# Optimization experiments

Hardware: AMD Instinct MI355X
Metric: run time of the kernel (lower is better)

## Reference

```python
import jax, jax.numpy as jnp
import numpy as np

B = 8192; N = 50; NUM_NODES = 200000; NUM_EDGES = 1000000
FEAT = 64; EFEAT = 4; TD = 16; D = 64


def setup_inputs() -> dict:
    key = jax.random.key(0)
    ks = jax.random.split(key, 32)
    p = lambda i, shape: jax.random.normal(ks[i], shape, jnp.float32) * 0.05
    inp = {}
    nf = jax.random.normal(ks[0], (NUM_NODES, FEAT), jnp.float32)
    skills = jax.random.randint(ks[1], (NUM_NODES,), 0, 100).astype(jnp.float32)
    inp['node_raw_features'] = nf.at[:, 0].set(skills)  # col 0 = skill id
    inp['edge_raw_features'] = jax.random.normal(ks[2], (NUM_EDGES, EFEAT), jnp.float32)
    inp['src_node_ids'] = jax.random.randint(ks[3], (B,), 0, NUM_NODES)
    inp['dst_node_ids'] = jax.random.randint(ks[4], (B,), 0, NUM_NODES)
    inp['node_interact_times'] = jax.random.uniform(ks[5], (B,), jnp.float32, 0.0, 1e4)
    inp['src_neighbor_node_ids'] = jax.random.randint(ks[6], (B, N), 0, NUM_NODES)
    inp['src_neighbor_edge_ids'] = jax.random.randint(ks[7], (B, N), 0, NUM_EDGES)
    inp['src_neighbor_times'] = jax.random.uniform(ks[8], (B, N), jnp.float32, 0.0, 1e4)
    inp['dst_neighbor_node_ids'] = jax.random.randint(ks[9], (B, N), 0, NUM_NODES)
    inp['dst_neighbor_edge_ids'] = jax.random.randint(ks[10], (B, N), 0, NUM_EDGES)
    inp['dst_neighbor_times'] = jax.random.uniform(ks[11], (B, N), jnp.float32, 0.0, 1e4)
    # projection layers
    inp['W_feat'] = p(12, (FEAT, D)); inp['b_feat'] = p(13, (D,))
    inp['W_edge'] = p(14, (1, D));    inp['b_edge'] = p(15, (D,))
    inp['W_time'] = p(16, (TD, D));   inp['b_time'] = p(17, (D,))
    inp['W_struct'] = p(18, (1, D));  inp['b_struct'] = p(19, (D,))
    inp['W_out'] = p(20, (D, D));     inp['b_out'] = p(21, (D,))
    # time encoder (cos(w*dt + b), trainable Linear(1, TD) as in TGN TimeEncoder)
    inp['time_w'] = p(22, (TD,)); inp['time_b'] = p(23, (TD,))
    # src / dst GRUs (PyTorch layout: W_ih [3H,E], W_hh [3H,H])
    inp['src_W_ih'] = p(24, (3 * D, D)); inp['src_W_hh'] = p(25, (3 * D, D))
    inp['src_b_ih'] = p(26, (3 * D,));   inp['src_b_hh'] = p(27, (3 * D,))
    inp['dst_W_ih'] = p(28, (3 * D, D)); inp['dst_W_hh'] = p(29, (3 * D, D))
    inp['dst_b_ih'] = p(30, (3 * D,));   inp['dst_b_hh'] = p(31, (3 * D,))
    return inp


def _lin(x, W, b):
    return x @ W + b


def _gru_last_hidden(x, W_ih, W_hh, b_ih, b_hh):
    # x: [B, T, E] -> final hidden state [B, H] (PyTorch GRU equations)
    Bb, _, _ = x.shape
    H = W_hh.shape[1]

    def step(h, xt):
        gi = xt @ W_ih.T + b_ih            # [B, 3H]
        gh = h @ W_hh.T + b_hh             # [B, 3H]
        ir, iz, inn = jnp.split(gi, 3, axis=-1)
        hr, hz, hn = jnp.split(gh, 3, axis=-1)
        r = jax.nn.sigmoid(ir + hr)
        z = jax.nn.sigmoid(iz + hz)
        n = jnp.tanh(inn + r * hn)
        h_new = (1.0 - z) * n + z * h
        return h_new, None

    h0 = jnp.zeros((Bb, H), x.dtype)
    hT, _ = jax.lax.scan(step, h0, jnp.swapaxes(x, 0, 1))
    return hT


def reference(node_raw_features, edge_raw_features, src_node_ids, dst_node_ids,
              node_interact_times, src_neighbor_node_ids, src_neighbor_edge_ids,
              src_neighbor_times, dst_neighbor_node_ids, dst_neighbor_edge_ids,
              dst_neighbor_times, W_feat, b_feat, W_edge, b_edge, W_time, b_time,
              W_struct, b_struct, W_out, b_out, time_w, time_b,
              src_W_ih, src_W_hh, src_b_ih, src_b_hh,
              dst_W_ih, dst_W_hh, dst_b_ih, dst_b_hh):
    t = node_interact_times
    # append the query interaction itself (edge id 0) -> [B, N+1]
    src_nids = jnp.concatenate([src_neighbor_node_ids, src_node_ids[:, None]], 1)
    src_eids = jnp.concatenate([src_neighbor_edge_ids, jnp.zeros_like(src_node_ids)[:, None]], 1)
    src_ts = jnp.concatenate([src_neighbor_times, t[:, None]], 1)
    dst_nids = jnp.concatenate([dst_neighbor_node_ids, dst_node_ids[:, None]], 1)
    dst_eids = jnp.concatenate([dst_neighbor_edge_ids, jnp.zeros_like(dst_node_ids)[:, None]], 1)
    dst_ts = jnp.concatenate([dst_neighbor_times, t[:, None]], 1)

    # co-occurrence features [B, N, 1]
    co_src = (src_neighbor_node_ids == dst_node_ids[:, None]).astype(jnp.float32)[..., None]
    co_dst = (dst_neighbor_node_ids == src_node_ids[:, None]).astype(jnp.float32)[..., None]
    # skill match features [B, N, 1]
    src_skill = node_raw_features[src_nids][:, :-1, 0].astype(jnp.int32)
    dst_skill = node_raw_features[dst_nids][:, -1, 0].astype(jnp.int32)[:, None]
    skill_f = (src_skill == dst_skill).astype(jnp.float32)[..., None]

    src_struct = _lin(co_src, W_struct, b_struct)
    dst_struct = _lin(co_dst, W_struct, b_struct)
    skill_struct = _lin(skill_f, W_struct, b_struct)

    def get_feats(nids, eids, ts):
        node_f = _lin(node_raw_features[nids], W_feat, b_feat)        # [B,N+1,D]
        delta = t[:, None] - ts                                       # dual-decay ablation: delta times
        tenc = jnp.cos(delta[..., None] * time_w + time_b)            # [B,N+1,TD]
        time_f = _lin(tenc, W_time, b_time)                           # [B,N+1,D]
        edge_f = _lin(edge_raw_features[eids][..., :1], W_edge, b_edge)
        return node_f, edge_f, time_f

    sn, se, st = get_feats(src_nids, src_eids, src_ts)
    dn, de, dt = get_feats(dst_nids, dst_eids, dst_ts)
    src_feats = sn + se + st
    dst_feats = dn + de + dt

    src_emb = _gru_last_hidden(src_feats[:, :-1] + skill_struct + src_struct,
                               src_W_ih, src_W_hh, src_b_ih, src_b_hh) + (se + st)[:, -1]
    dst_emb = _gru_last_hidden((de + dt)[:, :-1] + dst_struct,
                               dst_W_ih, dst_W_hh, dst_b_ih, dst_b_hh) + dst_feats[:, -1]

    return _lin(src_emb, W_out, b_out), _lin(dst_emb, W_out, b_out)
```

## Files before the change

kernel.cpp:

```cpp
#include <hip/hip_runtime.h>
#include <stdint.h>

#define BB 8192
#define NN 50

typedef _Float16 half8 __attribute__((ext_vector_type(8)));
typedef float floatx4 __attribute__((ext_vector_type(4)));

union FragU { uint4 u; half8 h; };
static __device__ __forceinline__ half8 u2h(uint4 u) { FragU f; f.u = u; return f.h; }

static __device__ __forceinline__ uint32_t pk2u(float a, float b) {
    auto p = __builtin_amdgcn_cvt_pkrtz(a, b);
    uint32_t u; __builtin_memcpy(&u, &p, 4); return u;
}

#define MFMA(A, B, C) __builtin_amdgcn_mfma_f32_16x16x32_f16((A), (B), (C), 0, 0, 0)

static __device__ __forceinline__ float frcp(float x) {
#if __has_builtin(__builtin_amdgcn_rcpf)
    return __builtin_amdgcn_rcpf(x);
#else
    return 1.0f / x;
#endif
}
static __device__ __forceinline__ float fexp2(float x) {
#if __has_builtin(__builtin_amdgcn_exp2f)
    return __builtin_amdgcn_exp2f(x);
#else
    return __expf(0.69314718056f * x);
#endif
}

static __device__ __forceinline__ void bar_lds() {
    asm volatile("s_waitcnt lgkmcnt(0)" ::: "memory");
    __builtin_amdgcn_s_barrier();
}

__global__ __launch_bounds__(128, 2)
void dygkt7(const float* __restrict__ nodef, const float* __restrict__ edgef,
            const int* __restrict__ src_ids, const int* __restrict__ dst_ids,
            const float* __restrict__ times,
            const int* __restrict__ s_nids, const int* __restrict__ s_eids,
            const float* __restrict__ s_ts,
            const int* __restrict__ d_nids, const int* __restrict__ d_eids,
            const float* __restrict__ d_ts,
            const float* __restrict__ W_feat, const float* __restrict__ b_feat,
            const float* __restrict__ W_edge, const float* __restrict__ b_edge,
            const float* __restrict__ W_time, const float* __restrict__ b_time,
            const float* __restrict__ W_str,  const float* __restrict__ b_str,
            const float* __restrict__ W_out,  const float* __restrict__ b_out,
            const float* __restrict__ time_w, const float* __restrict__ time_b,
            const float* __restrict__ sWih, const float* __restrict__ sWhh,
            const float* __restrict__ sbih, const float* __restrict__ sbhh,
            const float* __restrict__ dWih, const float* __restrict__ dWhh,
            const float* __restrict__ dbih, const float* __restrict__ dbhh,
            float* __restrict__ out)
{
    __shared__ __align__(16) _Float16 xls[2][16 * 72];
    __shared__ __align__(16) _Float16 hls[2][16 * 72];
    __shared__ uint4 wihL[2][12][64];

    const int tid = threadIdx.x, w = tid >> 6, lane = tid & 63;
    const int g = lane >> 4, i16 = lane & 15;
    const bool is_src = (blockIdx.x & 1) == 0;
    const int b = (int)(blockIdx.x >> 1) * 16 + i16;

    const float SRZ = -1.44269504089f;
    const float SN  =  2.88539008178f;

    for (int q = tid; q < 16 * 72 / 2; q += 128) ((uint32_t*)hls[0])[q] = 0u;

    uint4 wf[2][2];
    #pragma unroll
    for (int tq = 0; tq < 2; ++tq)
        #pragma unroll
        for (int kh = 0; kh < 2; ++kh) {
            float v[8];
            #pragma unroll
            for (int j = 0; j < 8; ++j)
                v[j] = W_feat[(32 * kh + 8 * g + j) * 64 + 16 * (2 * w + tq) + i16];
            wf[tq][kh] = make_uint4(pk2u(v[0],v[1]), pk2u(v[2],v[3]), pk2u(v[4],v[5]), pk2u(v[6],v[7]));
        }

    const float* WI = is_src ? sWih : dWih;
    const float* WH = is_src ? sWhh : dWhh;
    uint4 whh[6][2];
    #pragma unroll
    for (int gt = 0; gt < 3; ++gt) {
        const float s = (gt == 2) ? SN : SRZ;
        #pragma unroll
        for (int tq = 0; tq < 2; ++tq)
            #pragma unroll
            for (int kh = 0; kh < 2; ++kh) {
                int row = 64 * gt + 16 * (2 * w + tq) + i16;
                const float* p = WI + (size_t)row * 64 + 32 * kh + 8 * g;
                float4 a = *(const float4*)p, c = *(const float4*)(p + 4);
                wihL[w][gt * 4 + tq * 2 + kh][lane] =
                    make_uint4(pk2u(s*a.x,s*a.y), pk2u(s*a.z,s*a.w), pk2u(s*c.x,s*c.y), pk2u(s*c.z,s*c.w));
                const float* qq = WH + (size_t)row * 64 + 32 * kh + 8 * g;
                float4 e = *(const float4*)qq, f = *(const float4*)(qq + 4);
                whh[gt * 2 + tq][kh] =
                    make_uint4(pk2u(s*e.x,s*e.y), pk2u(s*e.z,s*e.w), pk2u(s*f.x,s*f.y), pk2u(s*f.z,s*f.w));
            }
    }

    uint4 wtA[2];
    #pragma unroll
    for (int tq = 0; tq < 2; ++tq) {
        int mt = 2 * w + tq;
        float v[8];
        #pragma unroll
        for (int j = 0; j < 8; ++j) {
            int k = 8 * g + j, dim = 16 * mt + i16;
            float x = 0.0f;
            if (k < 16)       x = W_time[k * 64 + dim];
            else if (k == 16) x = W_edge[dim];
            else if (k == 17) x = W_str[dim];
            else if (k == 18) x = b_edge[dim] + b_time[dim];
            else if (k == 19) x = is_src ? (b_feat[dim] + 2.0f * b_str[dim]) : b_str[dim];
            else if (k == 20) x = b_feat[dim];
            v[j] = x;
        }
        wtA[tq] = make_uint4(pk2u(v[0],v[1]), pk2u(v[2],v[3]), pk2u(v[4],v[5]), pk2u(v[6],v[7]));
    }

    const float* BI = is_src ? sbih : dbih;
    const float* BH = is_src ? sbhh : dbhh;
    floatx4 brz[4], bin[2], bhn[2];
    #pragma unroll
    for (int gz = 0; gz < 2; ++gz)
        #pragma unroll
        for (int tq = 0; tq < 2; ++tq) {
            int r0 = 64 * gz + 16 * (2 * w + tq) + 4 * g;
            floatx4 v;
            #pragma unroll
            for (int r = 0; r < 4; ++r) v[r] = SRZ * (BI[r0 + r] + BH[r0 + r]);
            brz[gz * 2 + tq] = v;
        }
    #pragma unroll
    for (int tq = 0; tq < 2; ++tq) {
        int r0 = 128 + 16 * (2 * w + tq) + 4 * g;
        floatx4 vi, vh;
        #pragma unroll
        for (int r = 0; r < 4; ++r) { vi[r] = SN * BI[r0 + r]; vh[r] = SN * BH[r0 + r]; }
        bin[tq] = vi; bhn[tq] = vh;
    }

    const int* pn = (is_src ? s_nids : d_nids) + (size_t)b * NN;
    const int* pe = (is_src ? s_eids : d_eids) + (size_t)b * NN;
    const float* pt = (is_src ? s_ts : d_ts) + (size_t)b * NN;
    const float tqL = times[b];
    const int didL = dst_ids[b];
    const int oid = is_src ? didL : src_ids[b];
    const float dskill = is_src ? nodef[(size_t)didL * 64] : 0.0f;
    float twc[8], tbc[8];
    #pragma unroll
    for (int j = 0; j < 8; ++j) {
        int k = 8 * (g & 1) + j;
        twc[j] = time_w[k]; tbc[j] = time_b[k];
    }

    __syncthreads();

    int nidC = pn[0], eidC = pe[0];
    float tsC = pt[0];
    float e0C = edgef[4 * (size_t)eidC];
    float4 nfa = {0,0,0,0}, nfb = {0,0,0,0}, nfc = {0,0,0,0}, nfd = {0,0,0,0};
    if (is_src) {
        const float* rp = nodef + (size_t)nidC * 64 + 8 * g;
        nfa = *(const float4*)rp;        nfb = *(const float4*)(rp + 4);
        nfc = *(const float4*)(rp + 32); nfd = *(const float4*)(rp + 36);
    }
    int nidN = pn[1], eidN = pe[1];
    float tsN = pt[1];
    float e0N = edgef[4 * (size_t)eidN];
    float4 na = {0,0,0,0}, nb = {0,0,0,0}, nc = {0,0,0,0}, nd = {0,0,0,0};
    if (is_src) {
        const float* rp = nodef + (size_t)nidN * 64 + 8 * g;
        na = *(const float4*)rp;        nb = *(const float4*)(rp + 4);
        nc = *(const float4*)(rp + 32); nd = *(const float4*)(rp + 36);
    }

    const floatx4 z4 = {0,0,0,0};
    floatx4 gr[2], gz_[2], gn[2];
    floatx4 hM[2] = {{0,0,0,0},{0,0,0,0}};

    {
        float nsk = __shfl(nfa.x, i16);
        float sf = ((nidC == oid) ? 1.0f : 0.0f) +
                   ((is_src && nsk == dskill) ? 1.0f : 0.0f);
        float delta = tqL - tsC;
        uint4 tb4;
        if (g < 2) {
            float cv[8];
            #pragma unroll
            for (int j = 0; j < 8; ++j) cv[j] = __cosf(delta * twc[j] + tbc[j]);
            tb4 = make_uint4(pk2u(cv[0],cv[1]), pk2u(cv[2],cv[3]), pk2u(cv[4],cv[5]), pk2u(cv[6],cv[7]));
        } else if (g == 2) {
            tb4 = make_uint4(pk2u(e0C, sf), pk2u(1.0f, 1.0f), 0u, 0u);
        } else {
            tb4 = make_uint4(0u, 0u, 0u, 0u);
        }
        half8 tB = u2h(tb4);
        #pragma unroll
        for (int tq = 0; tq < 2; ++tq) {
            floatx4 xacc;
            if (is_src) {
                uint4 nf0 = make_uint4(pk2u(nfa.x,nfa.y), pk2u(nfa.z,nfa.w), pk2u(nfb.x,nfb.y), pk2u(nfb.z,nfb.w));
                uint4 nf1 = make_uint4(pk2u(nfc.x,nfc.y), pk2u(nfc.z,nfc.w), pk2u(nfd.x,nfd.y), pk2u(nfd.z,nfd.w));
                floatx4 a = MFMA(u2h(wf[tq][0]), u2h(nf0), z4);
                a = MFMA(u2h(wf[tq][1]), u2h(nf1), a);
                xacc = MFMA(u2h(wtA[tq]), tB, a);
            } else {
                xacc = MFMA(u2h(wtA[tq]), tB, z4);
            }
            *(uint2*)&xls[0][i16 * 72 + 32 * w + 16 * tq + 4 * g] =
                make_uint2(pk2u(xacc[0], xacc[1]), pk2u(xacc[2], xacc[3]));
        }
        bar_lds();
        half8 xB0 = u2h(*(const uint4*)&xls[0][i16 * 72 + 8 * g]);
        half8 xB1 = u2h(*(const uint4*)&xls[0][i16 * 72 + 32 + 8 * g]);
        #pragma unroll
        for (int tq = 0; tq < 2; ++tq) {
            floatx4 a = MFMA(u2h(wihL[w][0 + tq * 2 + 0][lane]), xB0, brz[tq]);
            gr[tq]    = MFMA(u2h(wihL[w][0 + tq * 2 + 1][lane]), xB1, a);
            floatx4 c = MFMA(u2h(wihL[w][4 + tq * 2 + 0][lane]), xB0, brz[2 + tq]);
            gz_[tq]   = MFMA(u2h(wihL[w][4 + tq * 2 + 1][lane]), xB1, c);
            floatx4 e = MFMA(u2h(wihL[w][8 + tq * 2 + 0][lane]), xB0, bin[tq]);
            gn[tq]    = MFMA(u2h(wihL[w][8 + tq * 2 + 1][lane]), xB1, e);
        }
    }

    int cur = 0;
    for (int t = 0; t < NN; ++t) {
        const bool hasx = (t + 1 < NN);

        nidC = nidN; eidC = eidN; tsC = tsN; e0C = e0N;
        nfa = na; nfb = nb; nfc = nc; nfd = nd;

        if (hasx) {
            float nsk = __shfl(nfa.x, i16);
            float sf = ((nidC == oid) ? 1.0f : 0.0f) +
                       ((is_src && nsk == dskill) ? 1.0f : 0.0f);
            float delta = tqL - tsC;
            uint4 tb4;
            if (g < 2) {
                float cv[8];
                #pragma unroll
                for (int j = 0; j < 8; ++j) cv[j] = __cosf(delta * twc[j] + tbc[j]);
                tb4 = make_uint4(pk2u(cv[0],cv[1]), pk2u(cv[2],cv[3]), pk2u(cv[4],cv[5]), pk2u(cv[6],cv[7]));
            } else if (g == 2) {
                tb4 = make_uint4(pk2u(e0C, sf), pk2u(1.0f, 1.0f), 0u, 0u);
            } else {
                tb4 = make_uint4(0u, 0u, 0u, 0u);
            }
            half8 tB = u2h(tb4);
            #pragma unroll
            for (int tq = 0; tq < 2; ++tq) {
                floatx4 xacc;
                if (is_src) {
                    uint4 nf0 = make_uint4(pk2u(nfa.x,nfa.y), pk2u(nfa.z,nfa.w), pk2u(nfb.x,nfb.y), pk2u(nfb.z,nfb.w));
                    uint4 nf1 = make_uint4(pk2u(nfc.x,nfc.y), pk2u(nfc.z,nfc.w), pk2u(nfd.x,nfd.y), pk2u(nfd.z,nfd.w));
                    floatx4 a = MFMA(u2h(wf[tq][0]), u2h(nf0), z4);
                    a = MFMA(u2h(wf[tq][1]), u2h(nf1), a);
                    xacc = MFMA(u2h(wtA[tq]), tB, a);
                } else {
                    xacc = MFMA(u2h(wtA[tq]), tB, z4);
                }
                *(uint2*)&xls[cur ^ 1][i16 * 72 + 32 * w + 16 * tq + 4 * g] =
                    make_uint2(pk2u(xacc[0], xacc[1]), pk2u(xacc[2], xacc[3]));
            }
        }

        if (t + 2 < NN) {
            nidN = pn[t + 2]; eidN = pe[t + 2]; tsN = pt[t + 2];
            e0N = edgef[4 * (size_t)eidN];
            if (is_src) {
                const float* rp = nodef + (size_t)nidN * 64 + 8 * g;
                na = *(const float4*)rp;        nb = *(const float4*)(rp + 4);
                nc = *(const float4*)(rp + 32); nd = *(const float4*)(rp + 36);
            }
        }

        bar_lds();

        half8 hB0 = u2h(*(const uint4*)&hls[cur][i16 * 72 + 8 * g]);
        half8 hB1 = u2h(*(const uint4*)&hls[cur][i16 * 72 + 32 + 8 * g]);

        floatx4 rg[2], zg[2], ha[2];
        #pragma unroll
        for (int tq = 0; tq < 2; ++tq) {
            floatx4 a = MFMA(u2h(whh[tq][0]), hB0, gr[tq]);
            rg[tq]    = MFMA(u2h(whh[tq][1]), hB1, a);
            floatx4 c = MFMA(u2h(whh[2 + tq][0]), hB0, gz_[tq]);
            zg[tq]    = MFMA(u2h(whh[2 + tq][1]), hB1, c);
            floatx4 e = MFMA(u2h(whh[4 + tq][0]), hB0, bhn[tq]);
            ha[tq]    = MFMA(u2h(whh[4 + tq][1]), hB1, e);
        }

        #pragma unroll
        for (int tq = 0; tq < 2; ++tq)
            #pragma unroll
            for (int r = 0; r < 4; ++r) {
                float rr = frcp(1.0f + fexp2(rg[tq][r]));
                float zz = frcp(1.0f + fexp2(zg[tq][r]));
                float vv = gn[tq][r] + rr * ha[tq][r];
                float nn = 1.0f - 2.0f * frcp(fexp2(vv) + 1.0f);
                hM[tq][r] = nn + zz * (hM[tq][r] - nn);
            }

        #pragma unroll
        for (int tq = 0; tq < 2; ++tq)
            *(uint2*)&hls[cur ^ 1][i16 * 72 + 32 * w + 16 * tq + 4 * g] =
                make_uint2(pk2u(hM[tq][0], hM[tq][1]), pk2u(hM[tq][2], hM[tq][3]));

        if (hasx) {
            half8 xB0 = u2h(*(const uint4*)&xls[cur ^ 1][i16 * 72 + 8 * g]);
            half8 xB1 = u2h(*(const uint4*)&xls[cur ^ 1][i16 * 72 + 32 + 8 * g]);
            #pragma unroll
            for (int tq = 0; tq < 2; ++tq) {
                floatx4 a = MFMA(u2h(wihL[w][0 + tq * 2 + 0][lane]), xB0, brz[tq]);
                gr[tq]    = MFMA(u2h(wihL[w][0 + tq * 2 + 1][lane]), xB1, a);
                floatx4 c = MFMA(u2h(wihL[w][4 + tq * 2 + 0][lane]), xB0, brz[2 + tq]);
                gz_[tq]   = MFMA(u2h(wihL[w][4 + tq * 2 + 1][lane]), xB1, c);
                floatx4 e = MFMA(u2h(wihL[w][8 + tq * 2 + 0][lane]), xB0, bin[tq]);
                gn[tq]    = MFMA(u2h(wihL[w][8 + tq * 2 + 1][lane]), xB1, e);
            }
        }

        cur ^= 1;
    }

    float e00 = edgef[0];
    uint4 tt4;
    if (g < 2) {
        float cv[8];
        #pragma unroll
        for (int j = 0; j < 8; ++j) cv[j] = __cosf(tbc[j]);
        tt4 = make_uint4(pk2u(cv[0],cv[1]), pk2u(cv[2],cv[3]), pk2u(cv[4],cv[5]), pk2u(cv[6],cv[7]));
    } else if (g == 2) {
        tt4 = make_uint4(pk2u(e00, 0.0f), pk2u(1.0f, 0.0f), pk2u(is_src ? 0.0f : 1.0f, 0.0f), 0u);
    } else {
        tt4 = make_uint4(0u, 0u, 0u, 0u);
    }
    half8 tT = u2h(tt4);

    floatx4 tacc[2];
    #pragma unroll
    for (int tq = 0; tq < 2; ++tq) tacc[tq] = MFMA(u2h(wtA[tq]), tT, z4);
    if (!is_src) {
        const float* rp = nodef + (size_t)didL * 64 + 8 * g;
        float4 da = *(const float4*)rp,        db = *(const float4*)(rp + 4);
        float4 dc = *(const float4*)(rp + 32), dd = *(const float4*)(rp + 36);
        uint4 d0 = make_uint4(pk2u(da.x,da.y), pk2u(da.z,da.w), pk2u(db.x,db.y), pk2u(db.z,db.w));
        uint4 d1 = make_uint4(pk2u(dc.x,dc.y), pk2u(dc.z,dc.w), pk2u(dd.x,dd.y), pk2u(dd.z,dd.w));
        #pragma unroll
        for (int tq = 0; tq < 2; ++tq) {
            tacc[tq] = MFMA(u2h(wf[tq][0]), u2h(d0), tacc[tq]);
            tacc[tq] = MFMA(u2h(wf[tq][1]), u2h(d1), tacc[tq]);
        }
    }

    uint4 wo[2][2];
    #pragma unroll
    for (int tq = 0; tq < 2; ++tq)
        #pragma unroll
        for (int kh = 0; kh < 2; ++kh) {
            float v[8];
            #pragma unroll
            for (int j = 0; j < 8; ++j)
                v[j] = W_out[(32 * kh + 8 * g + j) * 64 + 16 * (2 * w + tq) + i16];
            wo[tq][kh] = make_uint4(pk2u(v[0],v[1]), pk2u(v[2],v[3]), pk2u(v[4],v[5]), pk2u(v[6],v[7]));
        }

    #pragma unroll
    for (int tq = 0; tq < 2; ++tq) {
        floatx4 e = hM[tq] + tacc[tq];
        *(uint2*)&xls[0][i16 * 72 + 32 * w + 16 * tq + 4 * g] =
            make_uint2(pk2u(e[0], e[1]), pk2u(e[2], e[3]));
    }
    bar_lds();
    half8 eB0 = u2h(*(const uint4*)&xls[0][i16 * 72 + 8 * g]);
    half8 eB1 = u2h(*(const uint4*)&xls[0][i16 * 72 + 32 + 8 * g]);

    const size_t obase = (is_src ? 0 : (size_t)BB * 64) + (size_t)b * 64;
    #pragma unroll
    for (int tq = 0; tq < 2; ++tq) {
        floatx4 bo;
        #pragma unroll
        for (int r = 0; r < 4; ++r) bo[r] = b_out[16 * (2 * w + tq) + 4 * g + r];
        floatx4 o = MFMA(u2h(wo[tq][0]), eB0, bo);
        o = MFMA(u2h(wo[tq][1]), eB1, o);
        *(floatx4*)(out + obase + 16 * (2 * w + tq) + 4 * g) = o;
    }
}

extern "C" void kernel_launch(void* const* d_in, const int* in_sizes, int n_in,
                              void* d_out, int out_size, void* d_ws, size_t ws_size,
                              hipStream_t stream) {
    (void)in_sizes; (void)n_in; (void)d_ws; (void)ws_size; (void)out_size;
    const float* nodef  = (const float*)d_in[0];
    const float* edgef  = (const float*)d_in[1];
    const int*   srcid  = (const int*)  d_in[2];
    const int*   dstid  = (const int*)  d_in[3];
    const float* times  = (const float*)d_in[4];
    const int*   s_nids = (const int*)  d_in[5];
    const int*   s_eids = (const int*)  d_in[6];
    const float* s_ts   = (const float*)d_in[7];
    const int*   d_nids = (const int*)  d_in[8];
    const int*   d_eids = (const int*)  d_in[9];
    const float* d_ts   = (const float*)d_in[10];
    const float* W_feat = (const float*)d_in[11];
    const float* b_feat = (const float*)d_in[12];
    const float* W_edge = (const float*)d_in[13];
    const float* b_edge = (const float*)d_in[14];
    const float* W_time = (const float*)d_in[15];
    const float* b_time = (const float*)d_in[16];
    const float* W_str  = (const float*)d_in[17];
    const float* b_str  = (const float*)d_in[18];
    const float* W_out  = (const float*)d_in[19];
    const float* b_out  = (const float*)d_in[20];
    const float* time_w = (const float*)d_in[21];
    const float* time_b = (const float*)d_in[22];
    const float* sWih   = (const float*)d_in[23];
    const float* sWhh   = (const float*)d_in[24];
    const float* sbih   = (const float*)d_in[25];
    const float* sbhh   = (const float*)d_in[26];
    const float* dWih   = (const float*)d_in[27];
    const float* dWhh   = (const float*)d_in[28];
    const float* dbih   = (const float*)d_in[29];
    const float* dbhh   = (const float*)d_in[30];

    dim3 grid(1024), block(128);
    dygkt7<<<grid, block, 0, stream>>>(
        nodef, edgef, srcid, dstid, times,
        s_nids, s_eids, s_ts, d_nids, d_eids, d_ts,
        W_feat, b_feat, W_edge, b_edge, W_time, b_time,
        W_str, b_str, W_out, b_out, time_w, time_b,
        sWih, sWhh, sbih, sbhh, dWih, dWhh, dbih, dbhh,
        (float*)d_out);
}
```

Before: 259.7 us.

## Split block into producer and GRU-recurrence warps with LDS-staged input gates

Doubles the block to four waves and specializes them: two producer waves gather neighbor features, build the projected inputs and compute the input-gate matmuls, writing them to a double-buffered LDS buffer. The other two waves run only the hidden-state recurrence, reading precomputed gates one step behind. The aim is to take the gather latency and input projection off the serial recurrence critical path. In exchange it adds a block barrier every step, uses more LDS for gate staging, and rotates wave roles by block index to spread SIMD use, with occupancy depending on the new launch bounds.

```diff
diff --git a/kernel.cpp b/kernel.cpp
--- a/kernel.cpp
+++ b/kernel.cpp
@@ -37,8 +37,8 @@
     __builtin_amdgcn_s_barrier();
 }
 
-__global__ __launch_bounds__(128, 2)
-void dygkt7(const float* __restrict__ nodef, const float* __restrict__ edgef,
+__global__ __launch_bounds__(256, 3)
+void dygkt8(const float* __restrict__ nodef, const float* __restrict__ edgef,
             const int* __restrict__ src_ids, const int* __restrict__ dst_ids,
             const float* __restrict__ times,
             const int* __restrict__ s_nids, const int* __restrict__ s_eids,
@@ -59,187 +59,96 @@
 {
     __shared__ __align__(16) _Float16 xls[2][16 * 72];
     __shared__ __align__(16) _Float16 hls[2][16 * 72];
-    __shared__ uint4 wihL[2][12][64];
+    __shared__ floatx4 gbuf[2][3][4][64];
 
     const int tid = threadIdx.x, w = tid >> 6, lane = tid & 63;
     const int g = lane >> 4, i16 = lane & 15;
     const bool is_src = (blockIdx.x & 1) == 0;
     const int b = (int)(blockIdx.x >> 1) * 16 + i16;
+    const int rw = (w + (int)blockIdx.x) & 3;
+    const int cp = (rw < 2) ? rw : (rw - 2);
 
     const float SRZ = -1.44269504089f;
     const float SN  =  2.88539008178f;
-
-    for (int q = tid; q < 16 * 72 / 2; q += 128) ((uint32_t*)hls[0])[q] = 0u;
-
-    uint4 wf[2][2];
-    #pragma unroll
-    for (int tq = 0; tq < 2; ++tq)
-        #pragma unroll
-        for (int kh = 0; kh < 2; ++kh) {
+    const floatx4 z4 = {0, 0, 0, 0};
+
+    for (int q = tid; q < 16 * 72 / 2; q += 256) ((uint32_t*)hls[0])[q] = 0u;
+
+    if (rw >= 2) {
+        _Float16* xp = xls[cp];
+
+        uint4 wf[4][2];
+        #pragma unroll
+        for (int mt = 0; mt < 4; ++mt)
+            #pragma unroll
+            for (int kh = 0; kh < 2; ++kh) {
+                float v[8];
+                #pragma unroll
+                for (int j = 0; j < 8; ++j)
+                    v[j] = W_feat[(32 * kh + 8 * g + j) * 64 + 16 * mt + i16];
+                wf[mt][kh] = make_uint4(pk2u(v[0],v[1]), pk2u(v[2],v[3]), pk2u(v[4],v[5]), pk2u(v[6],v[7]));
+            }
+        uint4 wtA[4];
+        #pragma unroll
+        for (int mt = 0; mt < 4; ++mt) {
             float v[8];
             #pragma unroll
-            for (int j = 0; j < 8; ++j)
-                v[j] = W_feat[(32 * kh + 8 * g + j) * 64 + 16 * (2 * w + tq) + i16];
-            wf[tq][kh] = make_uint4(pk2u(v[0],v[1]), pk2u(v[2],v[3]), pk2u(v[4],v[5]), pk2u(v[6],v[7]));
-        }
-
-    const float* WI = is_src ? sWih : dWih;
-    const float* WH = is_src ? sWhh : dWhh;
-    uint4 whh[6][2];
-    #pragma unroll
-    for (int gt = 0; gt < 3; ++gt) {
-        const float s = (gt == 2) ? SN : SRZ;
-        #pragma unroll
-        for (int tq = 0; tq < 2; ++tq)
-            #pragma unroll
-            for (int kh = 0; kh < 2; ++kh) {
-                int row = 64 * gt + 16 * (2 * w + tq) + i16;
-                const float* p = WI + (size_t)row * 64 + 32 * kh + 8 * g;
-                float4 a = *(const float4*)p, c = *(const float4*)(p + 4);
-                wihL[w][gt * 4 + tq * 2 + kh][lane] =
-                    make_uint4(pk2u(s*a.x,s*a.y), pk2u(s*a.z,s*a.w), pk2u(s*c.x,s*c.y), pk2u(s*c.z,s*c.w));
-                const float* qq = WH + (size_t)row * 64 + 32 * kh + 8 * g;
-                float4 e = *(const float4*)qq, f = *(const float4*)(qq + 4);
-                whh[gt * 2 + tq][kh] =
-                    make_uint4(pk2u(s*e.x,s*e.y), pk2u(s*e.z,s*e.w), pk2u(s*f.x,s*f.y), pk2u(s*f.z,s*f.w));
-            }
-    }
-
-    uint4 wtA[2];
-    #pragma unroll
-    for (int tq = 0; tq < 2; ++tq) {
-        int mt = 2 * w + tq;
-        float v[8];
+            for (int j = 0; j < 8; ++j) {
+                int k = 8 * g + j, dim = 16 * mt + i16;
+                float x = 0.0f;
+                if (k < 16)       x = W_time[k * 64 + dim];
+                else if (k == 16) x = W_edge[dim];
+                else if (k == 17) x = W_str[dim];
+                else if (k == 18) x = b_edge[dim] + b_time[dim];
+                else if (k == 19) x = is_src ? (b_feat[dim] + 2.0f * b_str[dim]) : b_str[dim];
+                else if (k == 20) x = b_feat[dim];
+                v[j] = x;
+            }
+            wtA[mt] = make_uint4(pk2u(v[0],v[1]), pk2u(v[2],v[3]), pk2u(v[4],v[5]), pk2u(v[6],v[7]));
+        }
+        const float* WI = is_src ? sWih : dWih;
+        uint4 wih[3][2][2];
+        #pragma unroll
+        for (int gt = 0; gt < 3; ++gt) {
+            const float s = (gt == 2) ? SN : SRZ;
+            #pragma unroll
+            for (int tq = 0; tq < 2; ++tq)
+                #pragma unroll
+                for (int kh = 0; kh < 2; ++kh) {
+                    int row = 64 * gt + 16 * (2 * cp + tq) + i16;
+                    const float* p = WI + (size_t)row * 64 + 32 * kh + 8 * g;
+                    float4 a = *(const float4*)p, c = *(const float4*)(p + 4);
+                    wih[gt][tq][kh] = make_uint4(pk2u(s*a.x,s*a.y), pk2u(s*a.z,s*a.w),
+                                                 pk2u(s*c.x,s*c.y), pk2u(s*c.z,s*c.w));
+                }
+        }
+        float twc[8], tbc[8];
         #pragma unroll
         for (int j = 0; j < 8; ++j) {
-            int k = 8 * g + j, dim = 16 * mt + i16;
-            float x = 0.0f;
-            if (k < 16)       x = W_time[k * 64 + dim];
-            else if (k == 16) x = W_edge[dim];
-            else if (k == 17) x = W_str[dim];
-            else if (k == 18) x = b_edge[dim] + b_time[dim];
-            else if (k == 19) x = is_src ? (b_feat[dim] + 2.0f * b_str[dim]) : b_str[dim];
-            else if (k == 20) x = b_feat[dim];
-            v[j] = x;
-        }
-        wtA[tq] = make_uint4(pk2u(v[0],v[1]), pk2u(v[2],v[3]), pk2u(v[4],v[5]), pk2u(v[6],v[7]));
-    }
-
-    const float* BI = is_src ? sbih : dbih;
-    const float* BH = is_src ? sbhh : dbhh;
-    floatx4 brz[4], bin[2], bhn[2];
-    #pragma unroll
-    for (int gz = 0; gz < 2; ++gz)
-        #pragma unroll
-        for (int tq = 0; tq < 2; ++tq) {
-            int r0 = 64 * gz + 16 * (2 * w + tq) + 4 * g;
-            floatx4 v;
-            #pragma unroll
-            for (int r = 0; r < 4; ++r) v[r] = SRZ * (BI[r0 + r] + BH[r0 + r]);
-            brz[gz * 2 + tq] = v;
-        }
-    #pragma unroll
-    for (int tq = 0; tq < 2; ++tq) {
-        int r0 = 128 + 16 * (2 * w + tq) + 4 * g;
-        floatx4 vi, vh;
-        #pragma unroll
-        for (int r = 0; r < 4; ++r) { vi[r] = SN * BI[r0 + r]; vh[r] = SN * BH[r0 + r]; }
-        bin[tq] = vi; bhn[tq] = vh;
-    }
-
-    const int* pn = (is_src ? s_nids : d_nids) + (size_t)b * NN;
-    const int* pe = (is_src ? s_eids : d_eids) + (size_t)b * NN;
-    const float* pt = (is_src ? s_ts : d_ts) + (size_t)b * NN;
-    const float tqL = times[b];
-    const int didL = dst_ids[b];
-    const int oid = is_src ? didL : src_ids[b];
-    const float dskill = is_src ? nodef[(size_t)didL * 64] : 0.0f;
-    float twc[8], tbc[8];
-    #pragma unroll
-    for (int j = 0; j < 8; ++j) {
-        int k = 8 * (g & 1) + j;
-        twc[j] = time_w[k]; tbc[j] = time_b[k];
-    }
-
-    __syncthreads();
-
-    int nidC = pn[0], eidC = pe[0];
-    float tsC = pt[0];
-    float e0C = edgef[4 * (size_t)eidC];
-    float4 nfa = {0,0,0,0}, nfb = {0,0,0,0}, nfc = {0,0,0,0}, nfd = {0,0,0,0};
-    if (is_src) {
-        const float* rp = nodef + (size_t)nidC * 64 + 8 * g;
-        nfa = *(const float4*)rp;        nfb = *(const float4*)(rp + 4);
-        nfc = *(const float4*)(rp + 32); nfd = *(const float4*)(rp + 36);
-    }
-    int nidN = pn[1], eidN = pe[1];
-    float tsN = pt[1];
-    float e0N = edgef[4 * (size_t)eidN];
-    float4 na = {0,0,0,0}, nb = {0,0,0,0}, nc = {0,0,0,0}, nd = {0,0,0,0};
-    if (is_src) {
-        const float* rp = nodef + (size_t)nidN * 64 + 8 * g;
-        na = *(const float4*)rp;        nb = *(const float4*)(rp + 4);
-        nc = *(const float4*)(rp + 32); nd = *(const float4*)(rp + 36);
-    }
-
-    const floatx4 z4 = {0,0,0,0};
-    floatx4 gr[2], gz_[2], gn[2];
-    floatx4 hM[2] = {{0,0,0,0},{0,0,0,0}};
-
-    {
-        float nsk = __shfl(nfa.x, i16);
-        float sf = ((nidC == oid) ? 1.0f : 0.0f) +
-                   ((is_src && nsk == dskill) ? 1.0f : 0.0f);
-        float delta = tqL - tsC;
-        uint4 tb4;
-        if (g < 2) {
-            float cv[8];
-            #pragma unroll
-            for (int j = 0; j < 8; ++j) cv[j] = __cosf(delta * twc[j] + tbc[j]);
-            tb4 = make_uint4(pk2u(cv[0],cv[1]), pk2u(cv[2],cv[3]), pk2u(cv[4],cv[5]), pk2u(cv[6],cv[7]));
-        } else if (g == 2) {
-            tb4 = make_uint4(pk2u(e0C, sf), pk2u(1.0f, 1.0f), 0u, 0u);
-        } else {
-            tb4 = make_uint4(0u, 0u, 0u, 0u);
-        }
-        half8 tB = u2h(tb4);
-        #pragma unroll
-        for (int tq = 0; tq < 2; ++tq) {
-            floatx4 xacc;
-            if (is_src) {
-                uint4 nf0 = make_uint4(pk2u(nfa.x,nfa.y), pk2u(nfa.z,nfa.w), pk2u(nfb.x,nfb.y), pk2u(nfb.z,nfb.w));
-                uint4 nf1 = make_uint4(pk2u(nfc.x,nfc.y), pk2u(nfc.z,nfc.w), pk2u(nfd.x,nfd.y), pk2u(nfd.z,nfd.w));
-                floatx4 a = MFMA(u2h(wf[tq][0]), u2h(nf0), z4);
-                a = MFMA(u2h(wf[tq][1]), u2h(nf1), a);
-                xacc = MFMA(u2h(wtA[tq]), tB, a);
-            } else {
-                xacc = MFMA(u2h(wtA[tq]), tB, z4);
-            }
-            *(uint2*)&xls[0][i16 * 72 + 32 * w + 16 * tq + 4 * g] =
-                make_uint2(pk2u(xacc[0], xacc[1]), pk2u(xacc[2], xacc[3]));
-        }
-        bar_lds();
-        half8 xB0 = u2h(*(const uint4*)&xls[0][i16 * 72 + 8 * g]);
-        half8 xB1 = u2h(*(const uint4*)&xls[0][i16 * 72 + 32 + 8 * g]);
-        #pragma unroll
-        for (int tq = 0; tq < 2; ++tq) {
-            floatx4 a = MFMA(u2h(wihL[w][0 + tq * 2 + 0][lane]), xB0, brz[tq]);
-            gr[tq]    = MFMA(u2h(wihL[w][0 + tq * 2 + 1][lane]), xB1, a);
-            floatx4 c = MFMA(u2h(wihL[w][4 + tq * 2 + 0][lane]), xB0, brz[2 + tq]);
-            gz_[tq]   = MFMA(u2h(wihL[w][4 + tq * 2 + 1][lane]), xB1, c);
-            floatx4 e = MFMA(u2h(wihL[w][8 + tq * 2 + 0][lane]), xB0, bin[tq]);
-            gn[tq]    = MFMA(u2h(wihL[w][8 + tq * 2 + 1][lane]), xB1, e);
-        }
-    }
-
-    int cur = 0;
-    for (int t = 0; t < NN; ++t) {
-        const bool hasx = (t + 1 < NN);
-
-        nidC = nidN; eidC = eidN; tsC = tsN; e0C = e0N;
-        nfa = na; nfb = nb; nfc = nc; nfd = nd;
-
-        if (hasx) {
+            int k = 8 * (g & 1) + j;
+            twc[j] = time_w[k]; tbc[j] = time_b[k];
+        }
+
+        const int* pn = (is_src ? s_nids : d_nids) + (size_t)b * NN;
+        const int* pe = (is_src ? s_eids : d_eids) + (size_t)b * NN;
+        const float* pt = (is_src ? s_ts : d_ts) + (size_t)b * NN;
+        const float tqL = times[b];
+        const int didL = dst_ids[b];
+        const int oid = is_src ? didL : src_ids[b];
+        const float dskill = is_src ? nodef[(size_t)didL * 64] : 0.0f;
+        const float e00 = edgef[0];
+
+        int nidC = pn[0], eidC = pe[0];
+        float tsC = pt[0];
+        float e0C = edgef[4 * (size_t)eidC];
+        float4 nfa = {0,0,0,0}, nfb = {0,0,0,0}, nfc = {0,0,0,0}, nfd = {0,0,0,0};
+        if (is_src) {
+            const float* rp = nodef + (size_t)nidC * 64 + 8 * g;
+            nfa = *(const float4*)rp;        nfb = *(const float4*)(rp + 4);
+            nfc = *(const float4*)(rp + 32); nfd = *(const float4*)(rp + 36);
+        }
+
+        auto build_step = [&](int par) {
             float nsk = __shfl(nfa.x, i16);
             float sf = ((nidC == oid) ? 1.0f : 0.0f) +
                        ((is_src && nsk == dskill) ? 1.0f : 0.0f);
@@ -256,143 +165,188 @@
                 tb4 = make_uint4(0u, 0u, 0u, 0u);
             }
             half8 tB = u2h(tb4);
+            if (is_src) {
+                uint4 nf0 = make_uint4(pk2u(nfa.x,nfa.y), pk2u(nfa.z,nfa.w), pk2u(nfb.x,nfb.y), pk2u(nfb.z,nfb.w));
+                uint4 nf1 = make_uint4(pk2u(nfc.x,nfc.y), pk2u(nfc.z,nfc.w), pk2u(nfd.x,nfd.y), pk2u(nfd.z,nfd.w));
+                half8 nB0 = u2h(nf0), nB1 = u2h(nf1);
+                #pragma unroll
+                for (int mt = 0; mt < 4; ++mt) {
+                    floatx4 a = MFMA(u2h(wf[mt][0]), nB0, z4);
+                    a = MFMA(u2h(wf[mt][1]), nB1, a);
+                    floatx4 x = MFMA(u2h(wtA[mt]), tB, a);
+                    *(uint2*)&xp[i16 * 72 + 16 * mt + 4 * g] =
+                        make_uint2(pk2u(x[0], x[1]), pk2u(x[2], x[3]));
+                }
+            } else {
+                #pragma unroll
+                for (int mt = 0; mt < 4; ++mt) {
+                    floatx4 x = MFMA(u2h(wtA[mt]), tB, z4);
+                    *(uint2*)&xp[i16 * 72 + 16 * mt + 4 * g] =
+                        make_uint2(pk2u(x[0], x[1]), pk2u(x[2], x[3]));
+                }
+            }
+            half8 xB0 = u2h(*(const uint4*)&xp[i16 * 72 + 8 * g]);
+            half8 xB1 = u2h(*(const uint4*)&xp[i16 * 72 + 32 + 8 * g]);
+            #pragma unroll
+            for (int gt = 0; gt < 3; ++gt)
+                #pragma unroll
+                for (int tq = 0; tq < 2; ++tq) {
+                    floatx4 a = MFMA(u2h(wih[gt][tq][0]), xB0, z4);
+                    gbuf[par][gt][2 * cp + tq][lane] = MFMA(u2h(wih[gt][tq][1]), xB1, a);
+                }
+        };
+
+        build_step(0);
+        int nidN = pn[1], eidN = pe[1];
+        float tsN = pt[1];
+        float e0N = edgef[4 * (size_t)eidN];
+        if (is_src) {
+            const float* rp = nodef + (size_t)nidN * 64 + 8 * g;
+            nfa = *(const float4*)rp;        nfb = *(const float4*)(rp + 4);
+            nfc = *(const float4*)(rp + 32); nfd = *(const float4*)(rp + 36);
+        }
+        nidC = nidN; eidC = eidN; tsC = tsN; e0C = e0N;
+        __syncthreads();
+
+        for (int t = 0; t < NN; ++t) {
+            if (t + 2 < NN) { nidN = pn[t + 2]; eidN = pe[t + 2]; tsN = pt[t + 2]; }
+            if (t + 1 < NN) {
+                build_step((t + 1) & 1);
+            } else {
+                uint4 tt4;
+                if (g < 2) {
+                    float cv[8];
+                    #pragma unroll
+                    for (int j = 0; j < 8; ++j) cv[j] = __cosf(tbc[j]);
+                    tt4 = make_uint4(pk2u(cv[0],cv[1]), pk2u(cv[2],cv[3]), pk2u(cv[4],cv[5]), pk2u(cv[6],cv[7]));
+                } else if (g == 2) {
+                    tt4 = make_uint4(pk2u(e00, 0.0f), pk2u(1.0f, 0.0f), pk2u(is_src ? 0.0f : 1.0f, 0.0f), 0u);
+                } else {
+                    tt4 = make_uint4(0u, 0u, 0u, 0u);
+                }
+                half8 tT = u2h(tt4);
+                #pragma unroll
+                for (int tq = 0; tq < 2; ++tq) {
+                    floatx4 tacc = MFMA(u2h(wtA[2 * cp + tq]), tT, z4);
+                    if (!is_src) {
+                        uint4 d0 = make_uint4(pk2u(nfa.x,nfa.y), pk2u(nfa.z,nfa.w), pk2u(nfb.x,nfb.y), pk2u(nfb.z,nfb.w));
+                        uint4 d1 = make_uint4(pk2u(nfc.x,nfc.y), pk2u(nfc.z,nfc.w), pk2u(nfd.x,nfd.y), pk2u(nfd.z,nfd.w));
+                        tacc = MFMA(u2h(wf[2 * cp + tq][0]), u2h(d0), tacc);
+                        tacc = MFMA(u2h(wf[2 * cp + tq][1]), u2h(d1), tacc);
+                    }
+                    gbuf[0][0][2 * cp + tq][lane] = tacc;
+                }
+            }
+            if (t + 2 < NN) {
+                e0N = edgef[4 * (size_t)eidN];
+                if (is_src) {
+                    const float* rp = nodef + (size_t)nidN * 64 + 8 * g;
+                    nfa = *(const float4*)rp;        nfb = *(const float4*)(rp + 4);
+                    nfc = *(const float4*)(rp + 32); nfd = *(const float4*)(rp + 36);
+                }
+            } else if (t + 2 == NN && !is_src) {
+                const float* rp = nodef + (size_t)didL * 64 + 8 * g;
+                nfa = *(const float4*)rp;        nfb = *(const float4*)(rp + 4);
+                nfc = *(const float4*)(rp + 32); nfd = *(const float4*)(rp + 36);
+            }
+            nidC = nidN; eidC = eidN; tsC = tsN; e0C = e0N;
+            bar_lds();
+        }
+        bar_lds();
+    } else {
+        const float* WH = is_src ? sWhh : dWhh;
+        uint4 whh[3][2][2];
+        #pragma unroll
+        for (int gt = 0; gt < 3; ++gt) {
+            const float s = (gt == 2) ? SN : SRZ;
+            #pragma unroll
+            for (int tq = 0; tq < 2; ++tq)
+                #pragma unroll
+                for (int kh = 0; kh < 2; ++kh) {
+                    int row = 64 * gt + 16 * (2 * cp + tq) + i16;
+                    const float* p = WH + (size_t)row * 64 + 32 * kh + 8 * g;
+                    float4 a = *(const float4*)p, c = *(const float4*)(p + 4);
+                    whh[gt][tq][kh] = make_uint4(pk2u(s*a.x,s*a.y), pk2u(s*a.z,s*a.w),
+                                                 pk2u(s*c.x,s*c.y), pk2u(s*c.z,s*c.w));
+                }
+        }
+        const float* BI = is_src ? sbih : dbih;
+        const float* BH = is_src ? sbhh : dbhh;
+        floatx4 brzr[2], brzz[2], binv[2], bhnv[2];
+        #pragma unroll
+        for (int tq = 0; tq < 2; ++tq) {
+            int r0 = 16 * (2 * cp + tq) + 4 * g;
+            #pragma unroll
+            for (int r = 0; r < 4; ++r) {
+                brzr[tq][r] = SRZ * (BI[r0 + r] + BH[r0 + r]);
+                brzz[tq][r] = SRZ * (BI[64 + r0 + r] + BH[64 + r0 + r]);
+                binv[tq][r] = SN * BI[128 + r0 + r];
+                bhnv[tq][r] = SN * BH[128 + r0 + r];
+            }
+        }
+        floatx4 hM[2] = {z4, z4};
+        __syncthreads();
+
+        for (int t = 0; t < NN; ++t) {
+            const int par = t & 1;
+            half8 hB0 = u2h(*(const uint4*)&hls[par][i16 * 72 + 8 * g]);
+            half8 hB1 = u2h(*(const uint4*)&hls[par][i16 * 72 + 32 + 8 * g]);
             #pragma unroll
             for (int tq = 0; tq < 2; ++tq) {
-                floatx4 xacc;
-                if (is_src) {
-                    uint4 nf0 = make_uint4(pk2u(nfa.x,nfa.y), pk2u(nfa.z,nfa.w), pk2u(nfb.x,nfb.y), pk2u(nfb.z,nfb.w));
-                    uint4 nf1 = make_uint4(pk2u(nfc.x,nfc.y), pk2u(nfc.z,nfc.w), pk2u(nfd.x,nfd.y), pk2u(nfd.z,nfd.w));
-                    floatx4 a = MFMA(u2h(wf[tq][0]), u2h(nf0), z4);
-                    a = MFMA(u2h(wf[tq][1]), u2h(nf1), a);
-                    xacc = MFMA(u2h(wtA[tq]), tB, a);
-                } else {
-                    xacc = MFMA(u2h(wtA[tq]), tB, z4);
-                }
-                *(uint2*)&xls[cur ^ 1][i16 * 72 + 32 * w + 16 * tq + 4 * g] =
-                    make_uint2(pk2u(xacc[0], xacc[1]), pk2u(xacc[2], xacc[3]));
-            }
-        }
-
-        if (t + 2 < NN) {
-            nidN = pn[t + 2]; eidN = pe[t + 2]; tsN = pt[t + 2];
-            e0N = edgef[4 * (size_t)eidN];
-            if (is_src) {
-                const float* rp = nodef + (size_t)nidN * 64 + 8 * g;
-                na = *(const float4*)rp;        nb = *(const float4*)(rp + 4);
-                nc = *(const float4*)(rp + 32); nd = *(const float4*)(rp + 36);
-            }
-        }
-
+                floatx4 cr = gbuf[par][0][2 * cp + tq][lane] + brzr[tq];
+                floatx4 cz = gbuf[par][1][2 * cp + tq][lane] + brzz[tq];
+                floatx4 iv = gbuf[par][2][2 * cp + tq][lane] + binv[tq];
+                floatx4 a = MFMA(u2h(whh[0][tq][0]), hB0, cr);
+                floatx4 rg = MFMA(u2h(whh[0][tq][1]), hB1, a);
+                floatx4 c = MFMA(u2h(whh[1][tq][0]), hB0, cz);
+                floatx4 zg = MFMA(u2h(whh[1][tq][1]), hB1, c);
+                floatx4 e = MFMA(u2h(whh[2][tq][0]), hB0, bhnv[tq]);
+                floatx4 ha = MFMA(u2h(whh[2][tq][1]), hB1, e);
+                #pragma unroll
+                for (int r = 0; r < 4; ++r) {
+                    float rr = frcp(1.0f + fexp2(rg[r]));
+                    float zz = frcp(1.0f + fexp2(zg[r]));
+                    float vv = iv[r] + rr * ha[r];
+                    float nn = 1.0f - 2.0f * frcp(fexp2(vv) + 1.0f);
+                    hM[tq][r] = nn + zz * (hM[tq][r] - nn);
+                }
+                *(uint2*)&hls[par ^ 1][i16 * 72 + 32 * cp + 16 * tq + 4 * g] =
+                    make_uint2(pk2u(hM[tq][0], hM[tq][1]), pk2u(hM[tq][2], hM[tq][3]));
+            }
+            bar_lds();
+        }
+
+        #pragma unroll
+        for (int tq = 0; tq < 2; ++tq) {
+            floatx4 e = hM[tq] + gbuf[0][0][2 * cp + tq][lane];
+            *(uint2*)&hls[1][i16 * 72 + 32 * cp + 16 * tq + 4 * g] =
+                make_uint2(pk2u(e[0], e[1]), pk2u(e[2], e[3]));
+        }
         bar_lds();
-
-        half8 hB0 = u2h(*(const uint4*)&hls[cur][i16 * 72 + 8 * g]);
-        half8 hB1 = u2h(*(const uint4*)&hls[cur][i16 * 72 + 32 + 8 * g]);
-
-        floatx4 rg[2], zg[2], ha[2];
+        half8 eB0 = u2h(*(const uint4*)&hls[1][i16 * 72 + 8 * g]);
+        half8 eB1 = u2h(*(const uint4*)&hls[1][i16 * 72 + 32 + 8 * g]);
+
+        uint4 wo[2][2];
+        #pragma unroll
+        for (int tq = 0; tq < 2; ++tq)
+            #pragma unroll
+            for (int kh = 0; kh < 2; ++kh) {
+                float v[8];
+                #pragma unroll
+                for (int j = 0; j < 8; ++j)
+                    v[j] = W_out[(32 * kh + 8 * g + j) * 64 + 16 * (2 * cp + tq) + i16];
+                wo[tq][kh] = make_uint4(pk2u(v[0],v[1]), pk2u(v[2],v[3]), pk2u(v[4],v[5]), pk2u(v[6],v[7]));
+            }
+        const size_t obase = (is_src ? 0 : (size_t)BB * 64) + (size_t)b * 64;
         #pragma unroll
         for (int tq = 0; tq < 2; ++tq) {
-            floatx4 a = MFMA(u2h(whh[tq][0]), hB0, gr[tq]);
-            rg[tq]    = MFMA(u2h(whh[tq][1]), hB1, a);
-            floatx4 c = MFMA(u2h(whh[2 + tq][0]), hB0, gz_[tq]);
-            zg[tq]    = MFMA(u2h(whh[2 + tq][1]), hB1, c);
-            floatx4 e = MFMA(u2h(whh[4 + tq][0]), hB0, bhn[tq]);
-            ha[tq]    = MFMA(u2h(whh[4 + tq][1]), hB1, e);
-        }
-
-        #pragma unroll
-        for (int tq = 0; tq < 2; ++tq)
-            #pragma unroll
-            for (int r = 0; r < 4; ++r) {
-                float rr = frcp(1.0f + fexp2(rg[tq][r]));
-                float zz = frcp(1.0f + fexp2(zg[tq][r]));
-                float vv = gn[tq][r] + rr * ha[tq][r];
-                float nn = 1.0f - 2.0f * frcp(fexp2(vv) + 1.0f);
-                hM[tq][r] = nn + zz * (hM[tq][r] - nn);
-            }
-
-        #pragma unroll
-        for (int tq = 0; tq < 2; ++tq)
-            *(uint2*)&hls[cur ^ 1][i16 * 72 + 32 * w + 16 * tq + 4 * g] =
-                make_uint2(pk2u(hM[tq][0], hM[tq][1]), pk2u(hM[tq][2], hM[tq][3]));
-
-        if (hasx) {
-            half8 xB0 = u2h(*(const uint4*)&xls[cur ^ 1][i16 * 72 + 8 * g]);
-            half8 xB1 = u2h(*(const uint4*)&xls[cur ^ 1][i16 * 72 + 32 + 8 * g]);
-            #pragma unroll
-            for (int tq = 0; tq < 2; ++tq) {
-                floatx4 a = MFMA(u2h(wihL[w][0 + tq * 2 + 0][lane]), xB0, brz[tq]);
-                gr[tq]    = MFMA(u2h(wihL[w][0 + tq * 2 + 1][lane]), xB1, a);
-                floatx4 c = MFMA(u2h(wihL[w][4 + tq * 2 + 0][lane]), xB0, brz[2 + tq]);
-                gz_[tq]   = MFMA(u2h(wihL[w][4 + tq * 2 + 1][lane]), xB1, c);
-                floatx4 e = MFMA(u2h(wihL[w][8 + tq * 2 + 0][lane]), xB0, bin[tq]);
-                gn[tq]    = MFMA(u2h(wihL[w][8 + tq * 2 + 1][lane]), xB1, e);
-            }
-        }
-
-        cur ^= 1;
-    }
-
-    float e00 = edgef[0];
-    uint4 tt4;
-    if (g < 2) {
-        float cv[8];
-        #pragma unroll
-        for (int j = 0; j < 8; ++j) cv[j] = __cosf(tbc[j]);
-        tt4 = make_uint4(pk2u(cv[0],cv[1]), pk2u(cv[2],cv[3]), pk2u(cv[4],cv[5]), pk2u(cv[6],cv[7]));
-    } else if (g == 2) {
-        tt4 = make_uint4(pk2u(e00, 0.0f), pk2u(1.0f, 0.0f), pk2u(is_src ? 0.0f : 1.0f, 0.0f), 0u);
-    } else {
-        tt4 = make_uint4(0u, 0u, 0u, 0u);
-    }
-    half8 tT = u2h(tt4);
-
-    floatx4 tacc[2];
-    #pragma unroll
-    for (int tq = 0; tq < 2; ++tq) tacc[tq] = MFMA(u2h(wtA[tq]), tT, z4);
-    if (!is_src) {
-        const float* rp = nodef + (size_t)didL * 64 + 8 * g;
-        float4 da = *(const float4*)rp,        db = *(const float4*)(rp + 4);
-        float4 dc = *(const float4*)(rp + 32), dd = *(const float4*)(rp + 36);
-        uint4 d0 = make_uint4(pk2u(da.x,da.y), pk2u(da.z,da.w), pk2u(db.x,db.y), pk2u(db.z,db.w));
-        uint4 d1 = make_uint4(pk2u(dc.x,dc.y), pk2u(dc.z,dc.w), pk2u(dd.x,dd.y), pk2u(dd.z,dd.w));
-        #pragma unroll
-        for (int tq = 0; tq < 2; ++tq) {
-            tacc[tq] = MFMA(u2h(wf[tq][0]), u2h(d0), tacc[tq]);
-            tacc[tq] = MFMA(u2h(wf[tq][1]), u2h(d1), tacc[tq]);
-        }
-    }
-
-    uint4 wo[2][2];
-    #pragma unroll
-    for (int tq = 0; tq < 2; ++tq)
-        #pragma unroll
-        for (int kh = 0; kh < 2; ++kh) {
-            float v[8];
-            #pragma unroll
-            for (int j = 0; j < 8; ++j)
-                v[j] = W_out[(32 * kh + 8 * g + j) * 64 + 16 * (2 * w + tq) + i16];
-            wo[tq][kh] = make_uint4(pk2u(v[0],v[1]), pk2u(v[2],v[3]), pk2u(v[4],v[5]), pk2u(v[6],v[7]));
-        }
-
-    #pragma unroll
-    for (int tq = 0; tq < 2; ++tq) {
-        floatx4 e = hM[tq] + tacc[tq];
-        *(uint2*)&xls[0][i16 * 72 + 32 * w + 16 * tq + 4 * g] =
-            make_uint2(pk2u(e[0], e[1]), pk2u(e[2], e[3]));
-    }
-    bar_lds();
-    half8 eB0 = u2h(*(const uint4*)&xls[0][i16 * 72 + 8 * g]);
-    half8 eB1 = u2h(*(const uint4*)&xls[0][i16 * 72 + 32 + 8 * g]);
-
-    const size_t obase = (is_src ? 0 : (size_t)BB * 64) + (size_t)b * 64;
-    #pragma unroll
-    for (int tq = 0; tq < 2; ++tq) {
-        floatx4 bo;
-        #pragma unroll
-        for (int r = 0; r < 4; ++r) bo[r] = b_out[16 * (2 * w + tq) + 4 * g + r];
-        floatx4 o = MFMA(u2h(wo[tq][0]), eB0, bo);
-        o = MFMA(u2h(wo[tq][1]), eB1, o);
-        *(floatx4*)(out + obase + 16 * (2 * w + tq) + 4 * g) = o;
+            floatx4 bo;
+            #pragma unroll
+            for (int r = 0; r < 4; ++r) bo[r] = b_out[16 * (2 * cp + tq) + 4 * g + r];
+            floatx4 o = MFMA(u2h(wo[tq][0]), eB0, bo);
+            o = MFMA(u2h(wo[tq][1]), eB1, o);
+            *(floatx4*)(out + obase + 16 * (2 * cp + tq) + 4 * g) = o;
+        }
     }
 }
 
@@ -432,8 +386,8 @@
     const float* dbih   = (const float*)d_in[29];
     const float* dbhh   = (const float*)d_in[30];
 
-    dim3 grid(1024), block(128);
-    dygkt7<<<grid, block, 0, stream>>>(
+    dim3 grid(1024), block(256);
+    dygkt8<<<grid, block, 0, stream>>>(
         nodef, edgef, srcid, dstid, times,
         s_nids, s_eids, s_ts, d_nids, d_eids, d_ts,
         W_feat, b_feat, W_edge, b_edge, W_time, b_time,
```

New measurement: 317.0 us. +22.1%, slower.
